# Performance work log

Hardware: AMD Instinct MI355X
Metric: run time of the kernel (lower is better)

## Reference

```python
import jax, jax.numpy as jnp
import numpy as np

D_MODEL, N_GROUPS, N_EXPERTS = 512, 8, 8
TOP_K_L1, TOP_K_L2 = 2, 2
BATCH, SEQ = 2, 512


def setup_inputs() -> dict:
    key = jax.random.key(0)
    ks = jax.random.split(key, 6)
    d, G, E = D_MODEL, N_GROUPS, N_EXPERTS
    scale = 0.02
    x = jax.random.normal(ks[0], (BATCH, SEQ, d), dtype=jnp.float32)
    g1 = jax.random.normal(ks[1], (d, G), dtype=jnp.float32) * scale          # level-1 gate (no bias)
    g2 = jax.random.normal(ks[2], (G, d, E), dtype=jnp.float32) * scale       # per-group level-2 gate (no bias)
    W1 = jax.random.normal(ks[3], (G, E, d, 2 * d), dtype=jnp.float32) * scale
    b1 = jnp.zeros((G, E, 2 * d), dtype=jnp.float32)
    W2 = jax.random.normal(ks[4], (G, E, 2 * d, d), dtype=jnp.float32) * scale
    b2 = jnp.zeros((G, E, d), dtype=jnp.float32)
    return {"x": x, "g1": g1, "g2": g2, "W1": W1, "b1": b1, "W2": W2, "b2": b2}


def reference(x, g1, g2, W1, b1, W2, b2):
    B, S, d = x.shape
    G, E = g1.shape[1], g2.shape[2]
    xt = x.reshape(-1, d)  # [T, d]

    # ---- level-1 routing (groups) ----
    logits1 = xt @ g1                                   # [T, G]
    v1, i1 = jax.lax.top_k(logits1, TOP_K_L1)           # [T, k1]
    w1 = jax.nn.softmax(v1.astype(jnp.float32), axis=-1).astype(x.dtype)
    # dense combine weights: top-k indices are unique per token, so one-hot sum
    # is exactly the original gather/index_add_ math.
    c1 = jnp.sum(jax.nn.one_hot(i1, G, dtype=x.dtype) * w1[..., None], axis=1)  # [T, G]

    # ---- level-2 routing (experts within each group) ----
    logits2 = jnp.einsum('td,gde->tge', xt, g2)         # [T, G, E]
    v2, i2 = jax.lax.top_k(logits2, TOP_K_L2)           # [T, G, k2]
    w2 = jax.nn.softmax(v2.astype(jnp.float32), axis=-1).astype(x.dtype)
    c2 = jnp.sum(jax.nn.one_hot(i2, E, dtype=x.dtype) * w2[..., None], axis=2)  # [T, G, E]

    # ---- expert MLPs (Linear -> ReLU -> Linear), all experts, combined by weights ----
    h = jax.nn.relu(jnp.einsum('td,gedh->tgeh', xt, W1) + b1)   # [T, G, E, 2d]
    y = jnp.einsum('tgeh,gehd->tged', h, W2) + b2               # [T, G, E, d]

    group_out = jnp.einsum('tged,tge->tgd', y, c2)              # level-2 combine
    out = jnp.einsum('tgd,tg->td', group_out, c1)               # level-1 combine
    return out.reshape(B, S, d)
```

## Files before the change

kernel.cpp:

```cpp
#include <hip/hip_runtime.h>
#include <hip/hip_bf16.h>

#define D_M   512
#define H_M   1024
#define G_N   8
#define E_N   8
#define T_N   1024
#define NEXP  64
#define CAP   1024

#define KC    64
#define LDA   72

typedef __attribute__((ext_vector_type(8))) short bf16x8;
typedef __attribute__((ext_vector_type(4))) float f32x4;
typedef __attribute__((ext_vector_type(4))) unsigned int u32x4;

__device__ __forceinline__ unsigned short f2bf(float f) {
  unsigned u = __builtin_bit_cast(unsigned, f);
  u = (u + 0x7fffu + ((u >> 16) & 1u)) >> 16;
  return (unsigned short)u;
}
__device__ __forceinline__ unsigned pack2(float a, float b) {
  return (unsigned)f2bf(a) | ((unsigned)f2bf(b) << 16);
}

__global__ __launch_bounds__(64) void k_route(
    const float* __restrict__ x, const float* __restrict__ g1,
    const float* __restrict__ g2, int* __restrict__ slotGE,
    float* __restrict__ slotW) {
  __shared__ float xs[D_M];
  __shared__ float l2s[G_N][E_N];
  __shared__ float l1s[G_N];
  __shared__ float l1part[G_N][8];
  const int t = blockIdx.x;
  const int lane = threadIdx.x;
  const float* xr = x + (size_t)t * D_M;
  for (int i = lane; i < D_M; i += 64) xs[i] = xr[i];
  __syncthreads();
  {
    const int g = lane >> 3, e = lane & 7;
    const float* gp = g2 + (size_t)g * D_M * E_N + e;
    float acc = 0.f;
    #pragma unroll 8
    for (int i = 0; i < D_M; i++) acc += xs[i] * gp[(size_t)i * E_N];
    l2s[g][e] = acc;
  }
  {
    const int g = lane >> 3, c = lane & 7;
    float acc = 0.f;
    #pragma unroll 8
    for (int i = c * 64; i < c * 64 + 64; i++) acc += xs[i] * g1[(size_t)i * G_N + g];
    l1part[g][c] = acc;
  }
  __syncthreads();
  if (lane < G_N) {
    float s = 0.f;
    #pragma unroll
    for (int c = 0; c < 8; c++) s += l1part[lane][c];
    l1s[lane] = s;
  }
  __syncthreads();
  if (lane == 0) {
    int a1 = 0;
    for (int g = 1; g < G_N; g++) if (l1s[g] > l1s[a1]) a1 = g;
    int a2 = (a1 == 0) ? 1 : 0;
    for (int g = 0; g < G_N; g++) if (g != a1 && l1s[g] > l1s[a2]) a2 = g;
    const float m = l1s[a1];
    float w1a = __expf(l1s[a1] - m), w1b = __expf(l1s[a2] - m);
    const float inv = 1.f / (w1a + w1b);
    w1a *= inv; w1b *= inv;
    const int gsel[2] = {a1, a2};
    const float wsel[2] = {w1a, w1b};
    for (int a = 0; a < 2; a++) {
      const int g = gsel[a];
      int e1 = 0;
      for (int e = 1; e < E_N; e++) if (l2s[g][e] > l2s[g][e1]) e1 = e;
      int e2 = (e1 == 0) ? 1 : 0;
      for (int e = 0; e < E_N; e++) if (e != e1 && l2s[g][e] > l2s[g][e2]) e2 = e;
      const float mm = l2s[g][e1];
      float ua = __expf(l2s[g][e1] - mm), ub = __expf(l2s[g][e2] - mm);
      const float uin = 1.f / (ua + ub);
      ua *= uin; ub *= uin;
      slotGE[t * 4 + a * 2 + 0] = g * E_N + e1;
      slotW [t * 4 + a * 2 + 0] = wsel[a] * ua;
      slotGE[t * 4 + a * 2 + 1] = g * E_N + e2;
      slotW [t * 4 + a * 2 + 1] = wsel[a] * ub;
    }
  }
}

__global__ __launch_bounds__(256) void k_build(
    const int* __restrict__ slotGE, int* __restrict__ counts,
    int* __restrict__ list) {
  const int ts = blockIdx.x * 256 + threadIdx.x;
  if (ts >= T_N * 4) return;
  const int ge = slotGE[ts];
  const int pos = atomicAdd(&counts[ge], 1);
  list[ge * CAP + pos] = ts;
}

__global__ __launch_bounds__(256) void k_mlp1(
    const float* __restrict__ x, const float* __restrict__ W1,
    const float* __restrict__ b1, const int* __restrict__ counts,
    const int* __restrict__ list, unsigned short* __restrict__ h_ws) {
  const int ge = blockIdx.x >> 4;
  const int j0 = (blockIdx.x & 15) * 64;
  const int n = counts[ge];
  if (n == 0) return;
  __shared__ unsigned short xl[64 * LDA];
  __shared__ unsigned short wl[64 * LDA];
  __shared__ int tokTS[64];
  const int tid = threadIdx.x;
  const int lane = tid & 63, wave = tid >> 6;
  const int m16 = lane & 15, quad = lane >> 4;

  const int jp  = tid & 31;
  const int wko = (tid >> 5) & 7;
  const int tt  = tid & 63;
  const int xko = tid >> 6;

  const float* Wbase = W1 + (size_t)ge * D_M * H_M + j0 + jp * 2;
  float bv[4];
  #pragma unroll
  for (int nt = 0; nt < 4; nt++) bv[nt] = b1[ge * H_M + j0 + nt * 16 + m16];

  for (int t0 = 0; t0 < n; t0 += 64) {
    __syncthreads();
    if (tid < 64) {
      int idx = t0 + tid;
      tokTS[tid] = list[ge * CAP + (idx < n ? idx : 0)];
    }
    __syncthreads();
    const float* xrow = x + (size_t)(tokTS[tt] >> 2) * D_M;

    f32x4 acc[4] = {};
    float2 wreg[8];
    f32x4  xreg[4];

    {
      const float* wp = Wbase + (size_t)(wko * 8) * H_M;
      #pragma unroll
      for (int r = 0; r < 8; r++) wreg[r] = *(const float2*)(wp + (size_t)r * H_M);
      #pragma unroll
      for (int q = 0; q < 2; q++) {
        const int k = (xko + 4 * q) * 8;
        xreg[2*q+0] = *(const f32x4*)(xrow + k);
        xreg[2*q+1] = *(const f32x4*)(xrow + k + 4);
      }
    }
    #pragma unroll
    for (int c = 0; c < 8; c++) {
      __syncthreads();
      {
        u32x4 rlo = { pack2(wreg[0].x, wreg[1].x), pack2(wreg[2].x, wreg[3].x),
                      pack2(wreg[4].x, wreg[5].x), pack2(wreg[6].x, wreg[7].x) };
        u32x4 rhi = { pack2(wreg[0].y, wreg[1].y), pack2(wreg[2].y, wreg[3].y),
                      pack2(wreg[4].y, wreg[5].y), pack2(wreg[6].y, wreg[7].y) };
        *(u32x4*)&wl[(jp * 2 + 0) * LDA + wko * 8] = rlo;
        *(u32x4*)&wl[(jp * 2 + 1) * LDA + wko * 8] = rhi;
      }
      #pragma unroll
      for (int q = 0; q < 2; q++) {
        u32x4 xv = { pack2(xreg[2*q].x, xreg[2*q].y), pack2(xreg[2*q].z, xreg[2*q].w),
                     pack2(xreg[2*q+1].x, xreg[2*q+1].y), pack2(xreg[2*q+1].z, xreg[2*q+1].w) };
        *(u32x4*)&xl[tt * LDA + (xko + 4 * q) * 8] = xv;
      }
      __syncthreads();
      if (c < 7) {
        const int k0 = (c + 1) * KC;
        const float* wp = Wbase + (size_t)(k0 + wko * 8) * H_M;
        #pragma unroll
        for (int r = 0; r < 8; r++) wreg[r] = *(const float2*)(wp + (size_t)r * H_M);
        #pragma unroll
        for (int q = 0; q < 2; q++) {
          const int k = k0 + (xko + 4 * q) * 8;
          xreg[2*q+0] = *(const f32x4*)(xrow + k);
          xreg[2*q+1] = *(const f32x4*)(xrow + k + 4);
        }
      }
      #pragma unroll
      for (int kh = 0; kh < 2; kh++) {
        bf16x8 af = *(bf16x8*)&xl[(wave * 16 + m16) * LDA + kh * 32 + quad * 8];
        #pragma unroll
        for (int nt = 0; nt < 4; nt++) {
          bf16x8 bfr = *(bf16x8*)&wl[(nt * 16 + m16) * LDA + kh * 32 + quad * 8];
          acc[nt] = __builtin_amdgcn_mfma_f32_16x16x32_bf16(af, bfr, acc[nt], 0, 0, 0);
        }
      }
    }
    #pragma unroll
    for (int i = 0; i < 4; i++) {
      const int tr = wave * 16 + quad * 4 + i;
      if (t0 + tr < n) {
        const int ts = tokTS[tr];
        unsigned short* hp = h_ws + (size_t)ts * H_M + j0;
        #pragma unroll
        for (int nt = 0; nt < 4; nt++) {
          float v = acc[nt][i] + bv[nt];
          hp[nt * 16 + m16] = f2bf(v > 0.f ? v : 0.f);
        }
      }
    }
  }
}

__global__ __launch_bounds__(256) void k_mlp2(
    const unsigned short* __restrict__ h_ws, const float* __restrict__ W2,
    const float* __restrict__ b2, const int* __restrict__ counts,
    const int* __restrict__ list, const float* __restrict__ slotW,
    float* __restrict__ y_ws) {
  const int ge = blockIdx.x >> 3;
  const int j0 = (blockIdx.x & 7) * 64;
  const int n = counts[ge];
  if (n == 0) return;
  __shared__ unsigned short xl[64 * LDA];
  __shared__ unsigned short wl[64 * LDA];
  __shared__ int tokTS[64];
  const int tid = threadIdx.x;
  const int lane = tid & 63, wave = tid >> 6;
  const int m16 = lane & 15, quad = lane >> 4;

  const int jp  = tid & 31;
  const int wko = (tid >> 5) & 7;
  const int tt  = tid & 63;
  const int xko = tid >> 6;

  const float* Wbase = W2 + (size_t)ge * H_M * D_M + j0 + jp * 2;
  float bv[4];
  #pragma unroll
  for (int nt = 0; nt < 4; nt++) bv[nt] = b2[ge * D_M + j0 + nt * 16 + m16];

  for (int t0 = 0; t0 < n; t0 += 64) {
    __syncthreads();
    if (tid < 64) {
      int idx = t0 + tid;
      tokTS[tid] = list[ge * CAP + (idx < n ? idx : 0)];
    }
    __syncthreads();
    const unsigned short* hrow = h_ws + (size_t)tokTS[tt] * H_M;

    f32x4 acc[4] = {};
    float2 wreg[8];
    u32x4  hreg[2];

    {
      const float* wp = Wbase + (size_t)(wko * 8) * D_M;
      #pragma unroll
      for (int r = 0; r < 8; r++) wreg[r] = *(const float2*)(wp + (size_t)r * D_M);
      #pragma unroll
      for (int q = 0; q < 2; q++)
        hreg[q] = *(const u32x4*)(hrow + (xko + 4 * q) * 8);
    }
    #pragma unroll
    for (int c = 0; c < 16; c++) {
      __syncthreads();
      {
        u32x4 rlo = { pack2(wreg[0].x, wreg[1].x), pack2(wreg[2].x, wreg[3].x),
                      pack2(wreg[4].x, wreg[5].x), pack2(wreg[6].x, wreg[7].x) };
        u32x4 rhi = { pack2(wreg[0].y, wreg[1].y), pack2(wreg[2].y, wreg[3].y),
                      pack2(wreg[4].y, wreg[5].y), pack2(wreg[6].y, wreg[7].y) };
        *(u32x4*)&wl[(jp * 2 + 0) * LDA + wko * 8] = rlo;
        *(u32x4*)&wl[(jp * 2 + 1) * LDA + wko * 8] = rhi;
      }
      #pragma unroll
      for (int q = 0; q < 2; q++)
        *(u32x4*)&xl[tt * LDA + (xko + 4 * q) * 8] = hreg[q];
      __syncthreads();
      if (c < 15) {
        const int k0 = (c + 1) * KC;
        const float* wp = Wbase + (size_t)(k0 + wko * 8) * D_M;
        #pragma unroll
        for (int r = 0; r < 8; r++) wreg[r] = *(const float2*)(wp + (size_t)r * D_M);
        #pragma unroll
        for (int q = 0; q < 2; q++)
          hreg[q] = *(const u32x4*)(hrow + k0 + (xko + 4 * q) * 8);
      }
      #pragma unroll
      for (int kh = 0; kh < 2; kh++) {
        bf16x8 af = *(bf16x8*)&xl[(wave * 16 + m16) * LDA + kh * 32 + quad * 8];
        #pragma unroll
        for (int nt = 0; nt < 4; nt++) {
          bf16x8 bfr = *(bf16x8*)&wl[(nt * 16 + m16) * LDA + kh * 32 + quad * 8];
          acc[nt] = __builtin_amdgcn_mfma_f32_16x16x32_bf16(af, bfr, acc[nt], 0, 0, 0);
        }
      }
    }
    #pragma unroll
    for (int i = 0; i < 4; i++) {
      const int tr = wave * 16 + quad * 4 + i;
      if (t0 + tr < n) {
        const int ts = tokTS[tr];
        const float w = slotW[ts];
        float* yp = y_ws + (size_t)ts * D_M + j0;
        #pragma unroll
        for (int nt = 0; nt < 4; nt++)
          yp[nt * 16 + m16] = w * (acc[nt][i] + bv[nt]);
      }
    }
  }
}

__global__ __launch_bounds__(256) void k_combine(
    const float* __restrict__ y_ws, float* __restrict__ out) {
  const int idx = blockIdx.x * 256 + threadIdx.x;
  if (idx >= T_N * D_M / 4) return;
  const int t = idx >> 7;
  const int j = (idx & 127) * 4;
  const float* yp = y_ws + (size_t)t * 4 * D_M + j;
  const float4 a = *(const float4*)(yp);
  const float4 b = *(const float4*)(yp + D_M);
  const float4 c = *(const float4*)(yp + 2 * D_M);
  const float4 d = *(const float4*)(yp + 3 * D_M);
  float4 r;
  r.x = a.x + b.x + c.x + d.x;
  r.y = a.y + b.y + c.y + d.y;
  r.z = a.z + b.z + c.z + d.z;
  r.w = a.w + b.w + c.w + d.w;
  *(float4*)&out[(size_t)t * D_M + j] = r;
}

extern "C" void kernel_launch(void* const* d_in, const int* in_sizes, int n_in,
                              void* d_out, int out_size, void* d_ws, size_t ws_size,
                              hipStream_t stream) {
  const float* x  = (const float*)d_in[0];
  const float* g1 = (const float*)d_in[1];
  const float* g2 = (const float*)d_in[2];
  const float* W1 = (const float*)d_in[3];
  const float* b1 = (const float*)d_in[4];
  const float* W2 = (const float*)d_in[5];
  const float* b2 = (const float*)d_in[6];
  float* out = (float*)d_out;

  char* ws = (char*)d_ws;
  int*            slotGE = (int*)(ws + 0);
  float*          slotW  = (float*)(ws + 16384);
  int*            counts = (int*)(ws + 32768);
  int*            list   = (int*)(ws + 36864);
  unsigned short* h_ws   = (unsigned short*)(ws + 524288);
  float*          y_ws   = (float*)(ws + 524288 + 8388608);

  hipMemsetAsync(counts, 0, NEXP * sizeof(int), stream);
  k_route<<<T_N, 64, 0, stream>>>(x, g1, g2, slotGE, slotW);
  k_build<<<(T_N * 4) / 256, 256, 0, stream>>>(slotGE, counts, list);
  k_mlp1<<<NEXP * 16, 256, 0, stream>>>(x, W1, b1, counts, list, h_ws);
  k_mlp2<<<NEXP * 8, 256, 0, stream>>>(h_ws, W2, b2, counts, list, slotW, y_ws);
  k_combine<<<(T_N * D_M / 4) / 256, 256, 0, stream>>>(y_ws, out);
}
```

Before: 382.5 us.

## Stage full-K activations in LDS, stream weights into registers, split-K second MLP

Both expert MLP kernels now load the whole activation tile (64 tokens by 512 K) into LDS once per token chunk. Each wave then loads its weight column fragments straight from global memory into registers, converting to bf16 in flight, and prefetches the next K step. This removes the per-chunk LDS staging of weights and the barriers around it. mlp1 now uses 128-wide column tiles, and mlp2 splits K across two blocks that write separate partial buffers. The combine kernel sums the two partials and applies the routing weights. The cost is scattered per-lane fp32 weight loads with little coalescing, a larger LDS footprint that limits occupancy, and an extra partial-output buffer to read and write.

```diff
diff --git a/kernel.cpp b/kernel.cpp
--- a/kernel.cpp
+++ b/kernel.cpp
@@ -9,8 +9,7 @@
 #define NEXP  64
 #define CAP   1024
 
-#define KC    64
-#define LDA   72
+#define LDK   520
 
 typedef __attribute__((ext_vector_type(8))) short bf16x8;
 typedef __attribute__((ext_vector_type(4))) float f32x4;
@@ -100,223 +99,210 @@
   list[ge * CAP + pos] = ts;
 }
 
-__global__ __launch_bounds__(256) void k_mlp1(
+__global__ __launch_bounds__(256, 2) void k_mlp1(
     const float* __restrict__ x, const float* __restrict__ W1,
     const float* __restrict__ b1, const int* __restrict__ counts,
     const int* __restrict__ list, unsigned short* __restrict__ h_ws) {
-  const int ge = blockIdx.x >> 4;
-  const int j0 = (blockIdx.x & 15) * 64;
+  const int ge = blockIdx.x >> 3;
+  const int j0 = (blockIdx.x & 7) * 128;
   const int n = counts[ge];
   if (n == 0) return;
-  __shared__ unsigned short xl[64 * LDA];
-  __shared__ unsigned short wl[64 * LDA];
+  __shared__ unsigned short xl[64 * LDK];
   __shared__ int tokTS[64];
   const int tid = threadIdx.x;
   const int lane = tid & 63, wave = tid >> 6;
   const int m16 = lane & 15, quad = lane >> 4;
 
-  const int jp  = tid & 31;
-  const int wko = (tid >> 5) & 7;
-  const int tt  = tid & 63;
-  const int xko = tid >> 6;
-
-  const float* Wbase = W1 + (size_t)ge * D_M * H_M + j0 + jp * 2;
-  float bv[4];
+  const float* Wcol = W1 + (size_t)ge * (D_M * H_M) + j0 + wave * 32 + m16;
+  float bv[2];
   #pragma unroll
-  for (int nt = 0; nt < 4; nt++) bv[nt] = b1[ge * H_M + j0 + nt * 16 + m16];
+  for (int nt = 0; nt < 2; nt++) bv[nt] = b1[ge * H_M + j0 + wave * 32 + nt * 16 + m16];
 
   for (int t0 = 0; t0 < n; t0 += 64) {
     __syncthreads();
     if (tid < 64) {
       int idx = t0 + tid;
-      tokTS[tid] = list[ge * CAP + (idx < n ? idx : 0)];
-    }
-    __syncthreads();
-    const float* xrow = x + (size_t)(tokTS[tt] >> 2) * D_M;
-
-    f32x4 acc[4] = {};
-    float2 wreg[8];
-    f32x4  xreg[4];
-
+      tokTS[tid] = list[ge * CAP + (idx < n ? idx : n - 1)];
+    }
+    __syncthreads();
     {
-      const float* wp = Wbase + (size_t)(wko * 8) * H_M;
-      #pragma unroll
-      for (int r = 0; r < 8; r++) wreg[r] = *(const float2*)(wp + (size_t)r * H_M);
-      #pragma unroll
-      for (int q = 0; q < 2; q++) {
-        const int k = (xko + 4 * q) * 8;
-        xreg[2*q+0] = *(const f32x4*)(xrow + k);
-        xreg[2*q+1] = *(const f32x4*)(xrow + k + 4);
-      }
-    }
-    #pragma unroll
-    for (int c = 0; c < 8; c++) {
-      __syncthreads();
-      {
-        u32x4 rlo = { pack2(wreg[0].x, wreg[1].x), pack2(wreg[2].x, wreg[3].x),
-                      pack2(wreg[4].x, wreg[5].x), pack2(wreg[6].x, wreg[7].x) };
-        u32x4 rhi = { pack2(wreg[0].y, wreg[1].y), pack2(wreg[2].y, wreg[3].y),
-                      pack2(wreg[4].y, wreg[5].y), pack2(wreg[6].y, wreg[7].y) };
-        *(u32x4*)&wl[(jp * 2 + 0) * LDA + wko * 8] = rlo;
-        *(u32x4*)&wl[(jp * 2 + 1) * LDA + wko * 8] = rhi;
-      }
-      #pragma unroll
-      for (int q = 0; q < 2; q++) {
-        u32x4 xv = { pack2(xreg[2*q].x, xreg[2*q].y), pack2(xreg[2*q].z, xreg[2*q].w),
-                     pack2(xreg[2*q+1].x, xreg[2*q+1].y), pack2(xreg[2*q+1].z, xreg[2*q+1].w) };
-        *(u32x4*)&xl[tt * LDA + (xko + 4 * q) * 8] = xv;
-      }
-      __syncthreads();
-      if (c < 7) {
-        const int k0 = (c + 1) * KC;
-        const float* wp = Wbase + (size_t)(k0 + wko * 8) * H_M;
+      const int trow = tid >> 2;
+      const int kb = (tid & 3) * 4;
+      const float* xr = x + (size_t)(tokTS[trow] >> 2) * D_M + kb;
+      unsigned short* dst = &xl[trow * LDK + kb];
+      #pragma unroll 8
+      for (int rep = 0; rep < 32; rep++) {
+        f32x4 v = *(const f32x4*)(xr + rep * 16);
+        uint2 p = { pack2(v.x, v.y), pack2(v.z, v.w) };
+        *(uint2*)(dst + rep * 16) = p;
+      }
+    }
+    __syncthreads();
+
+    f32x4 acc[4][2] = {};
+    float bcur[2][8], bnxt[2][8];
+    #pragma unroll
+    for (int nt = 0; nt < 2; nt++)
+      #pragma unroll
+      for (int i = 0; i < 8; i++)
+        bcur[nt][i] = Wcol[(size_t)(quad * 8 + i) * H_M + nt * 16];
+
+    #pragma unroll 4
+    for (int s = 0; s < 16; s++) {
+      if (s < 15) {
         #pragma unroll
-        for (int r = 0; r < 8; r++) wreg[r] = *(const float2*)(wp + (size_t)r * H_M);
+        for (int nt = 0; nt < 2; nt++)
+          #pragma unroll
+          for (int i = 0; i < 8; i++)
+            bnxt[nt][i] = Wcol[(size_t)((s + 1) * 32 + quad * 8 + i) * H_M + nt * 16];
+      }
+      bf16x8 bf[2];
+      #pragma unroll
+      for (int nt = 0; nt < 2; nt++) {
+        u32x4 t = { pack2(bcur[nt][0], bcur[nt][1]), pack2(bcur[nt][2], bcur[nt][3]),
+                    pack2(bcur[nt][4], bcur[nt][5]), pack2(bcur[nt][6], bcur[nt][7]) };
+        bf[nt] = __builtin_bit_cast(bf16x8, t);
+      }
+      #pragma unroll
+      for (int mt = 0; mt < 4; mt++) {
+        bf16x8 af = *(bf16x8*)&xl[(mt * 16 + m16) * LDK + s * 32 + quad * 8];
+        acc[mt][0] = __builtin_amdgcn_mfma_f32_16x16x32_bf16(af, bf[0], acc[mt][0], 0, 0, 0);
+        acc[mt][1] = __builtin_amdgcn_mfma_f32_16x16x32_bf16(af, bf[1], acc[mt][1], 0, 0, 0);
+      }
+      #pragma unroll
+      for (int nt = 0; nt < 2; nt++)
         #pragma unroll
-        for (int q = 0; q < 2; q++) {
-          const int k = k0 + (xko + 4 * q) * 8;
-          xreg[2*q+0] = *(const f32x4*)(xrow + k);
-          xreg[2*q+1] = *(const f32x4*)(xrow + k + 4);
+        for (int i = 0; i < 8; i++) bcur[nt][i] = bnxt[nt][i];
+    }
+    #pragma unroll
+    for (int mt = 0; mt < 4; mt++)
+      #pragma unroll
+      for (int i = 0; i < 4; i++) {
+        const int tr = mt * 16 + quad * 4 + i;
+        if (t0 + tr < n) {
+          const int ts = tokTS[tr];
+          unsigned short* hp = h_ws + (size_t)ts * H_M + j0 + wave * 32 + m16;
+          #pragma unroll
+          for (int nt = 0; nt < 2; nt++) {
+            float v = acc[mt][nt][i] + bv[nt];
+            hp[nt * 16] = f2bf(v > 0.f ? v : 0.f);
+          }
         }
       }
-      #pragma unroll
-      for (int kh = 0; kh < 2; kh++) {
-        bf16x8 af = *(bf16x8*)&xl[(wave * 16 + m16) * LDA + kh * 32 + quad * 8];
-        #pragma unroll
-        for (int nt = 0; nt < 4; nt++) {
-          bf16x8 bfr = *(bf16x8*)&wl[(nt * 16 + m16) * LDA + kh * 32 + quad * 8];
-          acc[nt] = __builtin_amdgcn_mfma_f32_16x16x32_bf16(af, bfr, acc[nt], 0, 0, 0);
-        }
-      }
-    }
-    #pragma unroll
-    for (int i = 0; i < 4; i++) {
-      const int tr = wave * 16 + quad * 4 + i;
-      if (t0 + tr < n) {
-        const int ts = tokTS[tr];
-        unsigned short* hp = h_ws + (size_t)ts * H_M + j0;
-        #pragma unroll
-        for (int nt = 0; nt < 4; nt++) {
-          float v = acc[nt][i] + bv[nt];
-          hp[nt * 16 + m16] = f2bf(v > 0.f ? v : 0.f);
-        }
-      }
-    }
-  }
-}
-
-__global__ __launch_bounds__(256) void k_mlp2(
+  }
+}
+
+__global__ __launch_bounds__(256, 2) void k_mlp2(
     const unsigned short* __restrict__ h_ws, const float* __restrict__ W2,
     const float* __restrict__ b2, const int* __restrict__ counts,
-    const int* __restrict__ list, const float* __restrict__ slotW,
-    float* __restrict__ y_ws) {
+    const int* __restrict__ list, float* __restrict__ y0,
+    float* __restrict__ y1) {
   const int ge = blockIdx.x >> 3;
-  const int j0 = (blockIdx.x & 7) * 64;
+  const int j0 = ((blockIdx.x >> 1) & 3) * 128;
+  const int ks = blockIdx.x & 1;
   const int n = counts[ge];
   if (n == 0) return;
-  __shared__ unsigned short xl[64 * LDA];
-  __shared__ unsigned short wl[64 * LDA];
+  __shared__ unsigned short xl[64 * LDK];
   __shared__ int tokTS[64];
   const int tid = threadIdx.x;
   const int lane = tid & 63, wave = tid >> 6;
   const int m16 = lane & 15, quad = lane >> 4;
 
-  const int jp  = tid & 31;
-  const int wko = (tid >> 5) & 7;
-  const int tt  = tid & 63;
-  const int xko = tid >> 6;
-
-  const float* Wbase = W2 + (size_t)ge * H_M * D_M + j0 + jp * 2;
-  float bv[4];
+  const float* Wcol = W2 + (size_t)ge * (H_M * D_M) + (size_t)(ks * 512) * D_M + j0 + wave * 32 + m16;
+  float bv[2];
   #pragma unroll
-  for (int nt = 0; nt < 4; nt++) bv[nt] = b2[ge * D_M + j0 + nt * 16 + m16];
+  for (int nt = 0; nt < 2; nt++)
+    bv[nt] = ks == 0 ? b2[ge * D_M + j0 + wave * 32 + nt * 16 + m16] : 0.f;
+  float* yk = ks == 0 ? y0 : y1;
 
   for (int t0 = 0; t0 < n; t0 += 64) {
     __syncthreads();
     if (tid < 64) {
       int idx = t0 + tid;
-      tokTS[tid] = list[ge * CAP + (idx < n ? idx : 0)];
-    }
-    __syncthreads();
-    const unsigned short* hrow = h_ws + (size_t)tokTS[tt] * H_M;
-
-    f32x4 acc[4] = {};
-    float2 wreg[8];
-    u32x4  hreg[2];
-
+      tokTS[tid] = list[ge * CAP + (idx < n ? idx : n - 1)];
+    }
+    __syncthreads();
     {
-      const float* wp = Wbase + (size_t)(wko * 8) * D_M;
-      #pragma unroll
-      for (int r = 0; r < 8; r++) wreg[r] = *(const float2*)(wp + (size_t)r * D_M);
-      #pragma unroll
-      for (int q = 0; q < 2; q++)
-        hreg[q] = *(const u32x4*)(hrow + (xko + 4 * q) * 8);
-    }
-    #pragma unroll
-    for (int c = 0; c < 16; c++) {
-      __syncthreads();
-      {
-        u32x4 rlo = { pack2(wreg[0].x, wreg[1].x), pack2(wreg[2].x, wreg[3].x),
-                      pack2(wreg[4].x, wreg[5].x), pack2(wreg[6].x, wreg[7].x) };
-        u32x4 rhi = { pack2(wreg[0].y, wreg[1].y), pack2(wreg[2].y, wreg[3].y),
-                      pack2(wreg[4].y, wreg[5].y), pack2(wreg[6].y, wreg[7].y) };
-        *(u32x4*)&wl[(jp * 2 + 0) * LDA + wko * 8] = rlo;
-        *(u32x4*)&wl[(jp * 2 + 1) * LDA + wko * 8] = rhi;
-      }
-      #pragma unroll
-      for (int q = 0; q < 2; q++)
-        *(u32x4*)&xl[tt * LDA + (xko + 4 * q) * 8] = hreg[q];
-      __syncthreads();
-      if (c < 15) {
-        const int k0 = (c + 1) * KC;
-        const float* wp = Wbase + (size_t)(k0 + wko * 8) * D_M;
+      const int trow = tid >> 2;
+      const int kb = (tid & 3) * 8;
+      const unsigned short* hr = h_ws + (size_t)tokTS[trow] * H_M + ks * 512 + kb;
+      unsigned short* dst = &xl[trow * LDK + kb];
+      #pragma unroll 8
+      for (int rep = 0; rep < 16; rep++)
+        *(u32x4*)(dst + rep * 32) = *(const u32x4*)(hr + rep * 32);
+    }
+    __syncthreads();
+
+    f32x4 acc[4][2] = {};
+    float bcur[2][8], bnxt[2][8];
+    #pragma unroll
+    for (int nt = 0; nt < 2; nt++)
+      #pragma unroll
+      for (int i = 0; i < 8; i++)
+        bcur[nt][i] = Wcol[(size_t)(quad * 8 + i) * D_M + nt * 16];
+
+    #pragma unroll 4
+    for (int s = 0; s < 16; s++) {
+      if (s < 15) {
         #pragma unroll
-        for (int r = 0; r < 8; r++) wreg[r] = *(const float2*)(wp + (size_t)r * D_M);
+        for (int nt = 0; nt < 2; nt++)
+          #pragma unroll
+          for (int i = 0; i < 8; i++)
+            bnxt[nt][i] = Wcol[(size_t)((s + 1) * 32 + quad * 8 + i) * D_M + nt * 16];
+      }
+      bf16x8 bf[2];
+      #pragma unroll
+      for (int nt = 0; nt < 2; nt++) {
+        u32x4 t = { pack2(bcur[nt][0], bcur[nt][1]), pack2(bcur[nt][2], bcur[nt][3]),
+                    pack2(bcur[nt][4], bcur[nt][5]), pack2(bcur[nt][6], bcur[nt][7]) };
+        bf[nt] = __builtin_bit_cast(bf16x8, t);
+      }
+      #pragma unroll
+      for (int mt = 0; mt < 4; mt++) {
+        bf16x8 af = *(bf16x8*)&xl[(mt * 16 + m16) * LDK + s * 32 + quad * 8];
+        acc[mt][0] = __builtin_amdgcn_mfma_f32_16x16x32_bf16(af, bf[0], acc[mt][0], 0, 0, 0);
+        acc[mt][1] = __builtin_amdgcn_mfma_f32_16x16x32_bf16(af, bf[1], acc[mt][1], 0, 0, 0);
+      }
+      #pragma unroll
+      for (int nt = 0; nt < 2; nt++)
         #pragma unroll
-        for (int q = 0; q < 2; q++)
-          hreg[q] = *(const u32x4*)(hrow + k0 + (xko + 4 * q) * 8);
-      }
-      #pragma unroll
-      for (int kh = 0; kh < 2; kh++) {
-        bf16x8 af = *(bf16x8*)&xl[(wave * 16 + m16) * LDA + kh * 32 + quad * 8];
-        #pragma unroll
-        for (int nt = 0; nt < 4; nt++) {
-          bf16x8 bfr = *(bf16x8*)&wl[(nt * 16 + m16) * LDA + kh * 32 + quad * 8];
-          acc[nt] = __builtin_amdgcn_mfma_f32_16x16x32_bf16(af, bfr, acc[nt], 0, 0, 0);
+        for (int i = 0; i < 8; i++) bcur[nt][i] = bnxt[nt][i];
+    }
+    #pragma unroll
+    for (int mt = 0; mt < 4; mt++)
+      #pragma unroll
+      for (int i = 0; i < 4; i++) {
+        const int tr = mt * 16 + quad * 4 + i;
+        if (t0 + tr < n) {
+          const int ts = tokTS[tr];
+          float* yp = yk + (size_t)ts * D_M + j0 + wave * 32 + m16;
+          #pragma unroll
+          for (int nt = 0; nt < 2; nt++)
+            yp[nt * 16] = acc[mt][nt][i] + bv[nt];
         }
       }
-    }
-    #pragma unroll
-    for (int i = 0; i < 4; i++) {
-      const int tr = wave * 16 + quad * 4 + i;
-      if (t0 + tr < n) {
-        const int ts = tokTS[tr];
-        const float w = slotW[ts];
-        float* yp = y_ws + (size_t)ts * D_M + j0;
-        #pragma unroll
-        for (int nt = 0; nt < 4; nt++)
-          yp[nt * 16 + m16] = w * (acc[nt][i] + bv[nt]);
-      }
-    }
   }
 }
 
 __global__ __launch_bounds__(256) void k_combine(
-    const float* __restrict__ y_ws, float* __restrict__ out) {
+    const float* __restrict__ y0, const float* __restrict__ y1,
+    const float* __restrict__ slotW, float* __restrict__ out) {
   const int idx = blockIdx.x * 256 + threadIdx.x;
   if (idx >= T_N * D_M / 4) return;
   const int t = idx >> 7;
   const int j = (idx & 127) * 4;
-  const float* yp = y_ws + (size_t)t * 4 * D_M + j;
-  const float4 a = *(const float4*)(yp);
-  const float4 b = *(const float4*)(yp + D_M);
-  const float4 c = *(const float4*)(yp + 2 * D_M);
-  const float4 d = *(const float4*)(yp + 3 * D_M);
-  float4 r;
-  r.x = a.x + b.x + c.x + d.x;
-  r.y = a.y + b.y + c.y + d.y;
-  r.z = a.z + b.z + c.z + d.z;
-  r.w = a.w + b.w + c.w + d.w;
+  float4 r = {0.f, 0.f, 0.f, 0.f};
+  #pragma unroll
+  for (int s = 0; s < 4; s++) {
+    const float w = slotW[t * 4 + s];
+    const size_t off = (size_t)(t * 4 + s) * D_M + j;
+    const float4 a = *(const float4*)(y0 + off);
+    const float4 b = *(const float4*)(y1 + off);
+    r.x += w * (a.x + b.x);
+    r.y += w * (a.y + b.y);
+    r.z += w * (a.z + b.z);
+    r.w += w * (a.w + b.w);
+  }
   *(float4*)&out[(size_t)t * D_M + j] = r;
 }
 
@@ -338,12 +324,13 @@
   int*            counts = (int*)(ws + 32768);
   int*            list   = (int*)(ws + 36864);
   unsigned short* h_ws   = (unsigned short*)(ws + 524288);
-  float*          y_ws   = (float*)(ws + 524288 + 8388608);
+  float*          y0     = (float*)(ws + 524288 + 8388608);
+  float*          y1     = (float*)(ws + 524288 + 16777216);
 
   hipMemsetAsync(counts, 0, NEXP * sizeof(int), stream);
   k_route<<<T_N, 64, 0, stream>>>(x, g1, g2, slotGE, slotW);
   k_build<<<(T_N * 4) / 256, 256, 0, stream>>>(slotGE, counts, list);
-  k_mlp1<<<NEXP * 16, 256, 0, stream>>>(x, W1, b1, counts, list, h_ws);
-  k_mlp2<<<NEXP * 8, 256, 0, stream>>>(h_ws, W2, b2, counts, list, slotW, y_ws);
-  k_combine<<<(T_N * D_M / 4) / 256, 256, 0, stream>>>(y_ws, out);
-}
+  k_mlp1<<<NEXP * 8, 256, 0, stream>>>(x, W1, b1, counts, list, h_ws);
+  k_mlp2<<<NEXP * 8, 256, 0, stream>>>(h_ws, W2, b2, counts, list, y0, y1);
+  k_combine<<<(T_N * D_M / 4) / 256, 256, 0, stream>>>(y0, y1, slotW, out);
+}
```

New measurement: 374.1 us. 2.2% less time.
